# Optimization experiments

Hardware: AMD Instinct MI355X
Metric: run time of the kernel (lower is better)

## Reference

```python
import jax, jax.numpy as jnp
import numpy as np
from math import sqrt as msqrt

D_MODEL, D_FF, N_HEADS, D_K, D_V = 1024, 4096, 16, 64, 64
NEG = -1e9

def gelu_erf(x):
    return 0.5 * x * (1.0 + jax.lax.erf(x / msqrt(2.0)))

def layer_norm(x, g, b, eps=1e-5):
    mu = jnp.mean(x, axis=-1, keepdims=True)
    var = jnp.mean(jnp.square(x - mu), axis=-1, keepdims=True)
    return (x - mu) * jax.lax.rsqrt(var + eps) * g + b

def setup_inputs() -> dict:
    key = jax.random.key(0)
    ks = jax.random.split(key, 12)
    B, S = 2, 2048
    s = lambda fan_in: 1.0 / msqrt(fan_in)
    inp = {
        "x": jax.random.normal(ks[0], (B, S, D_MODEL), dtype=jnp.float32),
        "pad_mask": jnp.zeros((B, S, S), dtype=bool),
        "W_Q": jax.random.uniform(ks[1], (D_MODEL, N_HEADS * D_K), minval=-s(D_MODEL), maxval=s(D_MODEL)),
        "W_K": jax.random.uniform(ks[2], (D_MODEL, N_HEADS * D_K), minval=-s(D_MODEL), maxval=s(D_MODEL)),
        "W_V": jax.random.uniform(ks[3], (D_MODEL, N_HEADS * D_V), minval=-s(D_MODEL), maxval=s(D_MODEL)),
        "W_O": jax.random.uniform(ks[4], (N_HEADS * D_V, D_MODEL), minval=-s(N_HEADS * D_V), maxval=s(N_HEADS * D_V)),
        "fc1_w": jax.random.uniform(ks[5], (D_MODEL, D_FF), minval=-s(D_MODEL), maxval=s(D_MODEL)),
        "fc1_b": jax.random.uniform(ks[6], (D_FF,), minval=-s(D_MODEL), maxval=s(D_MODEL)),
        "fc2_w": jax.random.uniform(ks[7], (D_FF, D_MODEL), minval=-s(D_FF), maxval=s(D_FF)),
        "fc2_b": jax.random.uniform(ks[8], (D_MODEL,), minval=-s(D_FF), maxval=s(D_FF)),
        "ln1_g": jnp.ones((D_MODEL,), jnp.float32),
        "ln1_b": jnp.zeros((D_MODEL,), jnp.float32),
        "ln2_g": jnp.ones((D_MODEL,), jnp.float32),
        "ln2_b": jnp.zeros((D_MODEL,), jnp.float32),
    }
    return inp

def reference(x, pad_mask, W_Q, W_K, W_V, W_O, fc1_w, fc1_b, fc2_w, fc2_b,
              ln1_g, ln1_b, ln2_g, ln2_b):
    B, S, _ = x.shape
    # --- pre-norm MHA ---
    residual = x
    h = layer_norm(x, ln1_g, ln1_b)
    q = (h @ W_Q).reshape(B, S, N_HEADS, D_K).transpose(0, 2, 1, 3)  # [B,H,S,dk]
    k = (h @ W_K).reshape(B, S, N_HEADS, D_K).transpose(0, 2, 1, 3)
    v = (h @ W_V).reshape(B, S, N_HEADS, D_V).transpose(0, 2, 1, 3)
    scores = jnp.einsum("bhqd,bhkd->bhqk", q, k) / msqrt(D_K)
    scores = jnp.where(pad_mask[:, None, :, :], NEG, scores)
    attn = jax.nn.softmax(scores, axis=-1)
    ctx = jnp.einsum("bhqk,bhkd->bhqd", attn, v)
    ctx = ctx.transpose(0, 2, 1, 3).reshape(B, S, N_HEADS * D_V)
    x = ctx @ W_O + residual
    # --- pre-norm FFN (dropout is identity at inference) ---
    residual = x
    h = layer_norm(x, ln2_g, ln2_b)
    h = gelu_erf(h @ fc1_w + fc1_b)
    x = h @ fc2_w + fc2_b + residual
    return x
```

## Files before the change

kernel.cpp:

```cpp
#include <hip/hip_runtime.h>
#include <hip/hip_bf16.h>
#include <math.h>

#define DI __device__ __forceinline__

typedef short s16x8 __attribute__((ext_vector_type(8)));
typedef unsigned short u16x8_t __attribute__((ext_vector_type(8)));
typedef float f32x4 __attribute__((ext_vector_type(4)));

static constexpr int T_TOK = 4096;
static constexpr int DM    = 1024;
static constexpr int DFF   = 4096;
static constexpr int S_LEN = 2048;
static constexpr int NB    = 2;
static constexpr int LDK   = 2048;

DI unsigned short f2bf(float f) {
    unsigned int u = __builtin_bit_cast(unsigned int, f);
    u += 0x7fffu + ((u >> 16) & 1u);
    return (unsigned short)(u >> 16);
}

DI unsigned pack_bf2(float a, float b) {
    unsigned ua = __builtin_bit_cast(unsigned, a) + 0x8000u;
    unsigned ub = __builtin_bit_cast(unsigned, b) + 0x8000u;
    return __builtin_amdgcn_perm(ub, ua, 0x07060302u);
}

DI float gelu_f(float x) {
    return 0.5f * x * (1.0f + erff(x * 0.70710678118654752440f));
}

DI int swz(int r) { return (r & 7) ^ ((r >> 3) & 7); }

DI void gload_lds16(const void* g, void* l) {
    __builtin_amdgcn_global_load_lds((const unsigned int*)g, (unsigned int*)l, 16, 0, 0);
}

__global__ __launch_bounds__(256) void tcvt_kernel(const float* __restrict__ in,
                                                   unsigned short* __restrict__ out,
                                                   int K, int N) {
    __shared__ float tile[32][33];
    const int tx = threadIdx.x & 31, ty = threadIdx.x >> 5;
    const int k0 = blockIdx.y * 32, n0 = blockIdx.x * 32;
#pragma unroll
    for (int i = 0; i < 4; ++i) {
        int k = ty + i * 8;
        tile[k][tx] = in[(size_t)(k0 + k) * N + n0 + tx];
    }
    __syncthreads();
#pragma unroll
    for (int i = 0; i < 4; ++i) {
        int n = ty + i * 8;
        out[(size_t)(n0 + n) * K + k0 + tx] = f2bf(tile[tx][n]);
    }
}

__global__ __launch_bounds__(256) void ln_kernel(const float* __restrict__ x,
                                                 const float* __restrict__ g,
                                                 const float* __restrict__ b,
                                                 unsigned short* __restrict__ out) {
    int row = blockIdx.x;
    int t = threadIdx.x;
    const float4 v = reinterpret_cast<const float4*>(x + (size_t)row * DM)[t];
    float s = v.x + v.y + v.z + v.w;
    float s2 = v.x * v.x + v.y * v.y + v.z * v.z + v.w * v.w;
#pragma unroll
    for (int m = 1; m < 64; m <<= 1) { s += __shfl_xor(s, m, 64); s2 += __shfl_xor(s2, m, 64); }
    __shared__ float red[8];
    int w = t >> 6;
    if ((t & 63) == 0) { red[w] = s; red[4 + w] = s2; }
    __syncthreads();
    s = red[0] + red[1] + red[2] + red[3];
    s2 = red[4] + red[5] + red[6] + red[7];
    float mu = s * (1.0f / DM);
    float var = s2 * (1.0f / DM) - mu * mu;
    float rs = rsqrtf(var + 1e-5f);
    float4 gv = reinterpret_cast<const float4*>(g)[t];
    float4 bv = reinterpret_cast<const float4*>(b)[t];
    ushort4 ov = make_ushort4(f2bf((v.x - mu) * rs * gv.x + bv.x),
                              f2bf((v.y - mu) * rs * gv.y + bv.y),
                              f2bf((v.z - mu) * rs * gv.z + bv.z),
                              f2bf((v.w - mu) * rs * gv.w + bv.w));
    reinterpret_cast<ushort4*>(out + (size_t)row * DM)[t] = ov;
}

template <int EPI, int BN>
__global__ __launch_bounds__(256) void gemm_kernel(const unsigned short* __restrict__ A,
                                                   const unsigned short* __restrict__ Bt,
                                                   const float* __restrict__ bias,
                                                   const float* __restrict__ resid,
                                                   void* __restrict__ Cv, void* __restrict__ Cv2,
                                                   int M, int N, int K) {
    constexpr int NN = BN / 32;
    constexpr int BCH = BN / 64;
    __shared__ unsigned short Asm[3][128][32];
    __shared__ unsigned short Bsm[3][BN][32];
    const int t = threadIdx.x, lane = t & 63, w = t >> 6;
    const int wr = w >> 1, wc = w & 1;
    const int m0 = blockIdx.y * 128, n0 = blockIdx.x * BN;
    const int c = lane & 15, g = lane >> 4;
    const int srow = lane >> 2, scol = (lane & 3) * 8;

    f32x4 acc[4][NN] = {};
    const unsigned short* Ab = A + (size_t)m0 * K;
    const unsigned short* Bb = Bt + (size_t)n0 * K;

    auto stage = [&](int buf, int k0) {
#pragma unroll
        for (int cc = 0; cc < 2; ++cc) {
            int ch = 2 * w + cc;
            int r = ch * 16 + srow;
            gload_lds16(Ab + (size_t)r * K + k0 + scol, &Asm[buf][ch * 16][0]);
        }
#pragma unroll
        for (int cc = 0; cc < BCH; ++cc) {
            int ch = BCH * w + cc;
            int r = ch * 16 + srow;
            gload_lds16(Bb + (size_t)r * K + k0 + scol, &Bsm[buf][ch * 16][0]);
        }
    };

    auto compute = [&](int buf) {
        s16x8 af[4], bf[NN];
#pragma unroll
        for (int i = 0; i < 4; ++i)
            af[i] = *reinterpret_cast<const s16x8*>(&Asm[buf][wr * 64 + i * 16 + c][g * 8]);
#pragma unroll
        for (int n = 0; n < NN; ++n)
            bf[n] = *reinterpret_cast<const s16x8*>(&Bsm[buf][wc * (BN / 2) + n * 16 + c][g * 8]);
#pragma unroll
        for (int i = 0; i < 4; ++i)
#pragma unroll
            for (int n = 0; n < NN; ++n)
                acc[i][n] = __builtin_amdgcn_mfma_f32_16x16x32_bf16(af[i], bf[n], acc[i][n], 0, 0, 0);
    };

    const int NK = K >> 5;
    stage(0, 0);
    stage(1, 32);
    int buf = 0;
    for (int i = 0; i < NK - 1; ++i) {
        if constexpr (BCH == 2) asm volatile("s_waitcnt vmcnt(4)" ::: "memory");
        else                    asm volatile("s_waitcnt vmcnt(3)" ::: "memory");
        __builtin_amdgcn_s_barrier();
        compute(buf);
        if (i + 2 < NK) {
            int nb = buf + 2; if (nb >= 3) nb -= 3;
            stage(nb, (i + 2) << 5);
        }
        ++buf; if (buf == 3) buf = 0;
    }
    asm volatile("s_waitcnt vmcnt(0)" ::: "memory");
    __builtin_amdgcn_s_barrier();
    compute(buf);

    const int crow = g * 4;
#pragma unroll
    for (int i = 0; i < 4; ++i) {
#pragma unroll
        for (int n = 0; n < NN; ++n) {
            const int col = n0 + wc * (BN / 2) + n * 16 + c;
#pragma unroll
            for (int j = 0; j < 4; ++j) {
                const int row = m0 + wr * 64 + i * 16 + crow + j;
                float v = acc[i][n][j];
                if constexpr (EPI == 2) {
                    v = gelu_f(v + bias[col]);
                    ((unsigned short*)Cv)[(size_t)row * N + col] = f2bf(v);
                } else if constexpr (EPI == 3) {
                    v = v + bias[col] + resid[(size_t)row * N + col];
                    ((float*)Cv)[(size_t)row * N + col] = v;
                } else if constexpr (EPI == 1) {
                    v = v + resid[(size_t)row * N + col];
                    ((float*)Cv)[(size_t)row * N + col] = v;
                } else {
                    if (col < 2048) {
                        float vv = (col < 1024) ? v * 0.125f : v;
                        ((unsigned short*)Cv)[(size_t)row * LDK + col] = f2bf(vv);
                    } else {
                        ((unsigned short*)Cv2)[(size_t)(col - 2048) * T_TOK + row] = f2bf(v);
                    }
                }
            }
        }
    }
}

__global__ __launch_bounds__(256) void attn_kernel(const unsigned short* __restrict__ QK,
                                                   const unsigned short* __restrict__ Vt,
                                                   const unsigned char* __restrict__ mask,
                                                   unsigned short* __restrict__ O) {
    const int qt = blockIdx.x, h = blockIdx.y, b = blockIdx.z;
    const int t = threadIdx.x, lane = t & 63, w = t >> 6;
    const int c = lane & 15, g = lane >> 4;
    const int crow = g * 4;
    const int qb0 = qt * 64;
    const int qw = qb0 + w * 16;
    const int swzc16 = swz(c) << 4;

    __shared__ unsigned short Ksm[2][64][64];
    __shared__ unsigned short Vsm[2][64][64];
    __shared__ unsigned short Psm[4][16][64];
    __shared__ unsigned char Msm[64][64];

    s16x8 qf[2];
    {
        const unsigned short* qp = QK + (size_t)(b * S_LEN + qw + c) * LDK + h * 64 + g * 8;
        qf[0] = *reinterpret_cast<const s16x8*>(qp);
        qf[1] = *reinterpret_cast<const s16x8*>(qp + 32);
    }

    float lsum = 0.f;
    f32x4 oacc[4] = {};

    const int vtok = t >> 2;
    const int vd0 = (t & 3) * 16;
    const unsigned char* mcol = mask + (size_t)b * S_LEN * S_LEN + (size_t)(qb0 + vtok) * S_LEN + vd0;
    const unsigned short* kg = QK + 1024;
    const int srow8 = lane >> 3, sslot = lane & 7;

    auto stage = [&](int buf, int kt) {
#pragma unroll
        for (int cc = 0; cc < 2; ++cc) {
            int ch = 2 * w + cc;
            int r = ch * 8 + srow8;
            int slot = sslot ^ swz(r);
            gload_lds16(kg + (size_t)(b * S_LEN + kt + r) * LDK + h * 64 + slot * 8,
                        &Ksm[buf][ch * 8][0]);
            gload_lds16(Vt + (size_t)(h * 64 + r) * T_TOK + b * S_LEN + kt + slot * 8,
                        &Vsm[buf][ch * 8][0]);
        }
    };

    stage(0, 0);
    uint4 mv0 = *reinterpret_cast<const uint4*>(mcol);
    asm volatile("s_waitcnt vmcnt(0)" ::: "memory");
    int anym = __syncthreads_or((mv0.x | mv0.y | mv0.z | mv0.w) != 0);
    if (anym) {
        *reinterpret_cast<uint4*>(&Msm[vtok][vd0]) = mv0;
        __syncthreads();
    }

    constexpr int NT = S_LEN / 64;
    for (int it = 0; it < NT; ++it) {
        const int cur = it & 1;
        uint4 mv = {0u, 0u, 0u, 0u};
        if (it < NT - 1) {
            stage(cur ^ 1, (it + 1) * 64);
            mv = *reinterpret_cast<const uint4*>(mcol + (it + 1) * 64);
        }

        f32x4 s[4] = {};
#pragma unroll
        for (int kh = 0; kh < 2; ++kh) {
#pragma unroll
            for (int kb = 0; kb < 4; ++kb) {
                int key = kb * 16 + c;
                int byte = key * 128 + (((kh * 4 + g) ^ swz(key)) << 4);
                s16x8 kf = *(const s16x8*)((const char*)&Ksm[cur][0][0] + byte);
                s[kb] = __builtin_amdgcn_mfma_f32_16x16x32_bf16(kf, qf[kh], s[kb], 0, 0, 0);
            }
        }
        if (anym) {
#pragma unroll
            for (int kb = 0; kb < 4; ++kb)
#pragma unroll
                for (int j = 0; j < 4; ++j)
                    if (Msm[w * 16 + c][kb * 16 + crow + j]) s[kb][j] = -1e9f;
        }

#pragma unroll
        for (int kb = 0; kb < 4; ++kb) {
            float p0 = __expf(s[kb][0]);
            float p1 = __expf(s[kb][1]);
            float p2 = __expf(s[kb][2]);
            float p3 = __expf(s[kb][3]);
            lsum += (p0 + p1) + (p2 + p3);
            uint2 pk = make_uint2(pack_bf2(p0, p1), pack_bf2(p2, p3));
            int byte = c * 128 + ((kb * 32 + g * 8) ^ swzc16);
            *(uint2*)((char*)&Psm[w][0][0] + byte) = pk;
        }

#pragma unroll
        for (int kh = 0; kh < 2; ++kh) {
            int pbyte = c * 128 + ((kh * 64 + g * 16) ^ swzc16);
            s16x8 pf = *(const s16x8*)((const char*)&Psm[w][0][0] + pbyte);
#pragma unroll
            for (int nb = 0; nb < 4; ++nb) {
                int d = nb * 16 + c;
                int byte = d * 128 + (((kh * 4 + g) ^ swz(d)) << 4);
                s16x8 vf = *(const s16x8*)((const char*)&Vsm[cur][0][0] + byte);
                oacc[nb] = __builtin_amdgcn_mfma_f32_16x16x32_bf16(pf, vf, oacc[nb], 0, 0, 0);
            }
        }

        asm volatile("s_waitcnt vmcnt(0)" ::: "memory");
        int nxt = __syncthreads_or((mv.x | mv.y | mv.z | mv.w) != 0);
        if (nxt) {
            *reinterpret_cast<uint4*>(&Msm[vtok][vd0]) = mv;
            __syncthreads();
        }
        anym = nxt;
    }

    lsum += __shfl_xor(lsum, 16);
    lsum += __shfl_xor(lsum, 32);
    float inv[4];
#pragma unroll
    for (int j = 0; j < 4; ++j) {
        float lq = __shfl(lsum, crow + j);
        inv[j] = lq > 0.f ? 1.0f / lq : 0.f;
    }
#pragma unroll
    for (int nb = 0; nb < 4; ++nb) {
#pragma unroll
        for (int j = 0; j < 4; ++j) {
            const size_t oo = (size_t)(b * S_LEN + qw + crow + j) * DM + h * 64 + nb * 16 + c;
            O[oo] = f2bf(oacc[nb][j] * inv[j]);
        }
    }
}

extern "C" void kernel_launch(void* const* d_in, const int* in_sizes, int n_in,
                              void* d_out, int out_size, void* d_ws, size_t ws_size,
                              hipStream_t stream) {
    (void)in_sizes; (void)n_in; (void)out_size; (void)ws_size;
    const float* x   = (const float*)d_in[0];
    const unsigned char* mask = (const unsigned char*)d_in[1];
    const float* WQ  = (const float*)d_in[2];
    const float* WK  = (const float*)d_in[3];
    const float* WV  = (const float*)d_in[4];
    const float* WO  = (const float*)d_in[5];
    const float* F1W = (const float*)d_in[6];
    const float* F1B = (const float*)d_in[7];
    const float* F2W = (const float*)d_in[8];
    const float* F2B = (const float*)d_in[9];
    const float* L1G = (const float*)d_in[10];
    const float* L1B = (const float*)d_in[11];
    const float* L2G = (const float*)d_in[12];
    const float* L2B = (const float*)d_in[13];
    float* out = (float*)d_out;

    char* ws = (char*)d_ws;
    size_t off = 0;
    auto alloc = [&](size_t bytes) -> void* {
        void* p = ws + off;
        off += (bytes + 255) & ~(size_t)255;
        return p;
    };
    unsigned short* h1    = (unsigned short*)alloc((size_t)T_TOK * DM * 2);
    unsigned short* qk    = (unsigned short*)alloc((size_t)T_TOK * LDK * 2);
    unsigned short* vt    = (unsigned short*)alloc((size_t)DM * T_TOK * 2);
    unsigned short* ctx   = (unsigned short*)alloc((size_t)T_TOK * DM * 2);
    float*          x2    = (float*)alloc((size_t)T_TOK * DM * 4);
    unsigned short* h2    = (unsigned short*)alloc((size_t)T_TOK * DM * 2);
    unsigned short* h3    = (unsigned short*)alloc((size_t)T_TOK * DFF * 2);
    unsigned short* WQKVt = (unsigned short*)alloc((size_t)3 * DM * DM * 2);
    unsigned short* WOt   = (unsigned short*)alloc((size_t)DM * DM * 2);
    unsigned short* F1Wt  = (unsigned short*)alloc((size_t)DFF * DM * 2);
    unsigned short* F2Wt  = (unsigned short*)alloc((size_t)DM * DFF * 2);

    dim3 t32(DM / 32, DM / 32);
    tcvt_kernel<<<t32, 256, 0, stream>>>(WQ, WQKVt, DM, DM);
    tcvt_kernel<<<t32, 256, 0, stream>>>(WK, WQKVt + (size_t)DM * DM, DM, DM);
    tcvt_kernel<<<t32, 256, 0, stream>>>(WV, WQKVt + (size_t)2 * DM * DM, DM, DM);
    tcvt_kernel<<<t32, 256, 0, stream>>>(WO, WOt, DM, DM);
    tcvt_kernel<<<dim3(DFF / 32, DM / 32), 256, 0, stream>>>(F1W, F1Wt, DM, DFF);
    tcvt_kernel<<<dim3(DM / 32, DFF / 32), 256, 0, stream>>>(F2W, F2Wt, DFF, DM);

    ln_kernel<<<T_TOK, 256, 0, stream>>>(x, L1G, L1B, h1);

    gemm_kernel<4, 128><<<dim3(3072 / 128, T_TOK / 128), 256, 0, stream>>>(
        h1, WQKVt, nullptr, nullptr, qk, vt, T_TOK, 3072, DM);

    attn_kernel<<<dim3(S_LEN / 64, 16, NB), 256, 0, stream>>>(qk, vt, mask, ctx);

    gemm_kernel<1, 64><<<dim3(DM / 64, T_TOK / 128), 256, 0, stream>>>(
        ctx, WOt, nullptr, x, x2, nullptr, T_TOK, DM, DM);

    ln_kernel<<<T_TOK, 256, 0, stream>>>(x2, L2G, L2B, h2);

    gemm_kernel<2, 128><<<dim3(DFF / 128, T_TOK / 128), 256, 0, stream>>>(
        h2, F1Wt, F1B, nullptr, h3, nullptr, T_TOK, DFF, DM);
    gemm_kernel<3, 64><<<dim3(DM / 64, T_TOK / 128), 256, 0, stream>>>(
        h3, F2Wt, F2B, x2, out, nullptr, T_TOK, DM, DFF);
}
```

Baseline: 457.1 us.

## Add 256x256-tile 8-wave GEMM with XCD-aware block remap for QKV and FC1

Adds a new GEMM kernel using 256x256 output tiles, 512 threads and a 64-wide K step. Each tile is held as four 128x128 quadrants in double-buffered, XOR-swizzled LDS, with direct global-to-LDS loads interleaved between quadrant MFMA phases and s_setprio raised around the MFMA blocks. Block IDs are remapped across the 8 XCDs to improve L2 locality. The QKV and FC1 projections now use this kernel to raise arithmetic intensity and overlap loads with compute. The tradeoff is fewer blocks (192 and 256 workgroups) at occupancy 1, which may leave compute units underfilled, and a complex hand-tuned wait and barrier schedule.

```diff
diff --git a/kernel.cpp b/kernel.cpp
--- a/kernel.cpp
+++ b/kernel.cpp
@@ -31,7 +31,7 @@
     return 0.5f * x * (1.0f + erff(x * 0.70710678118654752440f));
 }
 
-DI int swz(int r) { return (r & 7) ^ ((r >> 3) & 7); }
+DI int swz(int r) { return (r ^ (r >> 3)) & 7; }
 
 DI void gload_lds16(const void* g, void* l) {
     __builtin_amdgcn_global_load_lds((const unsigned int*)g, (unsigned int*)l, 16, 0, 0);
@@ -85,6 +85,145 @@
     reinterpret_cast<ushort4*>(out + (size_t)row * DM)[t] = ov;
 }
 
+template <int EPI>
+__global__ __launch_bounds__(512, 1) void gemm256_kernel(
+    const unsigned short* __restrict__ A,
+    const unsigned short* __restrict__ Bt,
+    const float* __restrict__ bias,
+    void* __restrict__ Cv, void* __restrict__ Cv2,
+    int M, int N, int K, int nbx) {
+    __shared__ unsigned short lds[2][2][256][64];
+    const int t = threadIdx.x, lane = t & 63, w = t >> 6;
+    const int wr = w >> 2, wc = w & 3;
+    const int c = lane & 15, g = lane >> 4;
+
+    const int nwg = gridDim.x;
+    const int bid = blockIdx.x;
+    const int sbid = (bid & 7) * (nwg >> 3) + (bid >> 3);
+    const int bx = sbid % nbx, by = sbid / nbx;
+    const int m0 = by * 256, n0 = bx * 256;
+
+    const int lrow = w * 8 + (lane >> 3);
+    const int lslot = lane & 7;
+    size_t aoff[2][2], boff[2][2];
+#pragma unroll
+    for (int gq = 0; gq < 2; ++gq)
+#pragma unroll
+        for (int ch = 0; ch < 2; ++ch) {
+            int rowp = gq * 128 + ch * 64 + lrow;
+            int slot = lslot ^ swz(rowp);
+            int am = m0 + ch * 128 + gq * 64 + lrow;
+            aoff[gq][ch] = (size_t)am * K * 2 + (size_t)slot * 16;
+            int inb = ch * 64 + lrow;
+            int bn = n0 + (inb >> 5) * 64 + gq * 32 + (inb & 31);
+            boff[gq][ch] = (size_t)bn * K * 2 + (size_t)slot * 16;
+        }
+
+    auto stgA = [&](int buf, int gq, int kt) {
+#pragma unroll
+        for (int ch = 0; ch < 2; ++ch)
+            gload_lds16((const char*)A + aoff[gq][ch] + (size_t)kt * 128,
+                        &lds[buf][0][gq * 128 + ch * 64 + w * 8][0]);
+    };
+    auto stgB = [&](int buf, int gq, int kt) {
+#pragma unroll
+        for (int ch = 0; ch < 2; ++ch)
+            gload_lds16((const char*)Bt + boff[gq][ch] + (size_t)kt * 128,
+                        &lds[buf][1][gq * 128 + ch * 64 + w * 8][0]);
+    };
+
+    f32x4 acc[8][4] = {};
+    struct Frags { s16x8 af[4][2]; s16x8 bf[2][2]; };
+
+    auto ldq = [&](int buf, int qm, int qn, Frags& f) {
+        const char* La = (const char*)&lds[buf][0][0][0];
+        const char* Lb = (const char*)&lds[buf][1][0][0];
+#pragma unroll
+        for (int mi = 0; mi < 4; ++mi) {
+            int row = qm * 128 + wr * 64 + mi * 16 + c;
+            int sw = swz(row);
+#pragma unroll
+            for (int k = 0; k < 2; ++k)
+                f.af[mi][k] = *(const s16x8*)(La + row * 128 + (((k << 2) + g) ^ sw) * 16);
+        }
+#pragma unroll
+        for (int ni = 0; ni < 2; ++ni) {
+            int row = qn * 128 + wc * 32 + ni * 16 + c;
+            int sw = swz(row);
+#pragma unroll
+            for (int k = 0; k < 2; ++k)
+                f.bf[ni][k] = *(const s16x8*)(Lb + row * 128 + (((k << 2) + g) ^ sw) * 16);
+        }
+    };
+    auto mmq = [&](int qm, int qn, const Frags& f) {
+        __builtin_amdgcn_s_setprio(1);
+#pragma unroll
+        for (int mi = 0; mi < 4; ++mi)
+#pragma unroll
+            for (int ni = 0; ni < 2; ++ni)
+#pragma unroll
+                for (int k = 0; k < 2; ++k)
+                    acc[qm * 4 + mi][qn * 2 + ni] = __builtin_amdgcn_mfma_f32_16x16x32_bf16(
+                        f.af[mi][k], f.bf[ni][k], acc[qm * 4 + mi][qn * 2 + ni], 0, 0, 0);
+        __builtin_amdgcn_s_setprio(0);
+    };
+
+#define BAR() __builtin_amdgcn_s_barrier()
+#define VM(N) asm volatile("s_waitcnt vmcnt(" #N ")" ::: "memory")
+
+    stgB(0, 0, 0); stgA(0, 0, 0); stgB(0, 1, 0); stgA(0, 1, 0);
+    stgB(1, 0, 1); stgA(1, 0, 1);
+    VM(0); BAR();
+
+    const int NI = K >> 7;
+    for (int it = 0; it < NI; ++it) {
+        const bool last = (it == NI - 1);
+        const int T0k = 2 * it, T1k = 2 * it + 1;
+        Frags f;
+        ldq(0, 0, 0, f); stgA(1, 1, T1k); BAR(); mmq(0, 0, f); VM(6); BAR();
+        ldq(1, 0, 0, f); stgB(1, 1, T1k); BAR(); mmq(0, 0, f); VM(6); BAR();
+        ldq(0, 1, 0, f); BAR(); mmq(1, 0, f);
+        if (last) { VM(0); } else { VM(2); }
+        BAR();
+        ldq(1, 1, 0, f); if (!last) stgB(0, 0, T0k + 2); BAR(); mmq(1, 0, f); VM(6); BAR();
+        ldq(0, 0, 1, f); if (!last) stgB(1, 0, T1k + 2); BAR(); mmq(0, 1, f);
+        if (last) { VM(0); } else { VM(4); }
+        BAR();
+        ldq(1, 0, 1, f); if (!last) stgA(0, 0, T0k + 2); BAR(); mmq(0, 1, f); BAR();
+        ldq(0, 1, 1, f); if (!last) stgA(1, 0, T1k + 2); BAR(); mmq(1, 1, f); BAR();
+        ldq(1, 1, 1, f);
+        if (!last) { stgA(0, 1, T0k + 2); stgB(0, 1, T0k + 2); }
+        BAR(); mmq(1, 1, f); VM(6); BAR();
+    }
+#undef BAR
+#undef VM
+
+#pragma unroll
+    for (int mi = 0; mi < 8; ++mi) {
+        const int rowb = m0 + wr * 128 + (mi >> 2) * 64 + (mi & 3) * 16 + g * 4;
+#pragma unroll
+        for (int ni = 0; ni < 4; ++ni) {
+            const int col = n0 + wc * 64 + (ni >> 1) * 32 + (ni & 1) * 16 + c;
+#pragma unroll
+            for (int j = 0; j < 4; ++j) {
+                const int row = rowb + j;
+                float v = acc[mi][ni][j];
+                if constexpr (EPI == 2) {
+                    v = gelu_f(v + bias[col]);
+                    ((unsigned short*)Cv)[(size_t)row * N + col] = f2bf(v);
+                } else {
+                    if (col < 2048) {
+                        float vv = (col < 1024) ? v * 0.125f : v;
+                        ((unsigned short*)Cv)[(size_t)row * LDK + col] = f2bf(vv);
+                    } else {
+                        ((unsigned short*)Cv2)[(size_t)(col - 2048) * T_TOK + row] = f2bf(v);
+                    }
+                }
+            }
+        }
+    }
+}
+
 template <int EPI, int BN>
 __global__ __launch_bounds__(256) void gemm_kernel(const unsigned short* __restrict__ A,
                                                    const unsigned short* __restrict__ Bt,
@@ -165,22 +304,12 @@
             for (int j = 0; j < 4; ++j) {
                 const int row = m0 + wr * 64 + i * 16 + crow + j;
                 float v = acc[i][n][j];
-                if constexpr (EPI == 2) {
-                    v = gelu_f(v + bias[col]);
-                    ((unsigned short*)Cv)[(size_t)row * N + col] = f2bf(v);
-                } else if constexpr (EPI == 3) {
+                if constexpr (EPI == 3) {
                     v = v + bias[col] + resid[(size_t)row * N + col];
                     ((float*)Cv)[(size_t)row * N + col] = v;
-                } else if constexpr (EPI == 1) {
+                } else {
                     v = v + resid[(size_t)row * N + col];
                     ((float*)Cv)[(size_t)row * N + col] = v;
-                } else {
-                    if (col < 2048) {
-                        float vv = (col < 1024) ? v * 0.125f : v;
-                        ((unsigned short*)Cv)[(size_t)row * LDK + col] = f2bf(vv);
-                    } else {
-                        ((unsigned short*)Cv2)[(size_t)(col - 2048) * T_TOK + row] = f2bf(v);
-                    }
                 }
             }
         }
@@ -371,8 +500,8 @@
 
     ln_kernel<<<T_TOK, 256, 0, stream>>>(x, L1G, L1B, h1);
 
-    gemm_kernel<4, 128><<<dim3(3072 / 128, T_TOK / 128), 256, 0, stream>>>(
-        h1, WQKVt, nullptr, nullptr, qk, vt, T_TOK, 3072, DM);
+    gemm256_kernel<4><<<(3072 / 256) * (T_TOK / 256), 512, 0, stream>>>(
+        h1, WQKVt, nullptr, qk, vt, T_TOK, 3072, DM, 3072 / 256);
 
     attn_kernel<<<dim3(S_LEN / 64, 16, NB), 256, 0, stream>>>(qk, vt, mask, ctx);
 
@@ -381,8 +510,9 @@
 
     ln_kernel<<<T_TOK, 256, 0, stream>>>(x2, L2G, L2B, h2);
 
-    gemm_kernel<2, 128><<<dim3(DFF / 128, T_TOK / 128), 256, 0, stream>>>(
-        h2, F1Wt, F1B, nullptr, h3, nullptr, T_TOK, DFF, DM);
+    gemm256_kernel<2><<<(DFF / 256) * (T_TOK / 256), 512, 0, stream>>>(
+        h2, F1Wt, F1B, h3, nullptr, T_TOK, DFF, DM, DFF / 256);
+
     gemm_kernel<3, 64><<<dim3(DM / 64, T_TOK / 128), 256, 0, stream>>>(
         h3, F2Wt, F2B, x2, out, nullptr, T_TOK, DM, DFF);
 }
```

After: 484.6 us. +6.0%, slower.
